# Optimization experiments

Hardware: AMD Instinct MI355X
Metric: run time of the kernel (lower is better)

The kernel has to match this reference:

```python
import jax, jax.numpy as jnp
import numpy as np

EMB = 2048
HEADS = 16


def setup_inputs() -> dict:
    key = jax.random.key(0)
    k_x, k_wqkv, k_bqkv, k_wo, k_bo = jax.random.split(key, 5)
    B, S, E = 2, 2048, EMB
    x = jax.random.normal(k_x, (B, S, E), dtype=jnp.float32)
    # nn.Linear weights stored as (in, out) for x @ W + b convention
    W_qkv = jax.random.normal(k_wqkv, (E, 3 * E), dtype=jnp.float32) * 0.02
    b_qkv = jax.random.normal(k_bqkv, (3 * E,), dtype=jnp.float32) * 0.02
    W_out = jax.random.normal(k_wo, (E, E), dtype=jnp.float32) * 0.02
    b_out = jax.random.normal(k_bo, (E,), dtype=jnp.float32) * 0.02
    return {"x": x, "W_qkv": W_qkv, "b_qkv": b_qkv, "W_out": W_out, "b_out": b_out}


def reference(x, W_qkv, b_qkv, W_out, b_out):
    B, S, E = x.shape
    H = HEADS
    dh = E // H
    # QKV projection: (B,S,3E)
    qkv = x @ W_qkv + b_qkv
    # Faithful to torch: reshape (B,S,H,3*dh) THEN split -> interleaved per-head q/k/v
    qkv = qkv.reshape(B, S, H, 3 * dh).transpose(0, 2, 1, 3)  # (B,H,S,3*dh)
    q, k, v = jnp.split(qkv, 3, axis=-1)  # each (B,H,S,dh)
    q = q / jnp.asarray(dh, q.dtype) ** 0.5
    scores = jnp.einsum('bhqd,bhkd->bhqk', q, k)  # (B,H,S,S)
    weights = jax.nn.softmax(scores, axis=-1)
    attn = jnp.einsum('bhqk,bhkd->bhqd', weights, v)  # (B,H,S,dh)
    attn = attn.transpose(0, 2, 1, 3).reshape(B, S, E)
    return attn @ W_out + b_out
```

## Files before the change

### kernel.cpp

```cpp
#include <hip/hip_runtime.h>
#include <type_traits>
#include <utility>

#define DI __device__ __forceinline__

typedef unsigned short u16;
typedef float f32x4 __attribute__((ext_vector_type(4)));
typedef float f32x16 __attribute__((ext_vector_type(16)));
typedef short s16x8 __attribute__((ext_vector_type(8)));
typedef __bf16 bf16x8 __attribute__((ext_vector_type(8)));

template <typename V, typename = void>
struct mfma_ok : std::false_type {};
template <typename V>
struct mfma_ok<V, std::void_t<decltype(__builtin_amdgcn_mfma_f32_16x16x32_bf16(
    std::declval<V>(), std::declval<V>(), std::declval<f32x4>(), 0, 0, 0))>>
    : std::true_type {};
using frag_t = std::conditional_t<mfma_ok<bf16x8>::value, bf16x8, s16x8>;

union U128 {
  int4 i;
  frag_t f;
  u16 s[8];
};

DI f32x4 mfma16(const U128& a, const U128& b, f32x4 c) {
  return __builtin_amdgcn_mfma_f32_16x16x32_bf16(a.f, b.f, c, 0, 0, 0);
}
DI f32x16 mfma32(const U128& a, const U128& b, f32x16 c) {
  return __builtin_amdgcn_mfma_f32_32x32x16_bf16(a.f, b.f, c, 0, 0, 0);
}

DI u16 f2b(float x) {
  union { float f; unsigned u; } v; v.f = x;
  unsigned r = v.u + 0x7FFFu + ((v.u >> 16) & 1u);
  return (u16)(r >> 16);
}

#if __has_builtin(__builtin_amdgcn_exp2f)
#define EXP2F __builtin_amdgcn_exp2f
#else
#define EXP2F exp2f
#endif

typedef __attribute__((address_space(1))) void gas_t;
typedef __attribute__((address_space(3))) void las_t;
DI void gll16(const void* g, void* l) {
  __builtin_amdgcn_global_load_lds((gas_t*)g, (las_t*)l, 16, 0, 0);
}

__global__ __launch_bounds__(256) void k_conv_bf16(const float* __restrict__ in,
                                                   u16* __restrict__ out, int n4) {
  int i = blockIdx.x * 256 + threadIdx.x;
  if (i >= n4) return;
  float4 v = ((const float4*)in)[i];
  ushort4 o;
  o.x = f2b(v.x); o.y = f2b(v.y); o.z = f2b(v.z); o.w = f2b(v.w);
  ((ushort4*)out)[i] = o;
}

__global__ __launch_bounds__(256) void k_transpose_f2b(const float* __restrict__ in,
                                                       u16* __restrict__ out,
                                                       int R, int C) {
  __shared__ __attribute__((aligned(16))) u16 Tb[64][68];
  int t = threadIdx.x;
  long r0 = (long)blockIdx.y * 64, c0 = (long)blockIdx.x * 64;
  int cq = (t & 15) * 4, rr = t >> 4;
#pragma unroll
  for (int it = 0; it < 4; ++it) {
    int r = rr + it * 16;
    float4 v = *(const float4*)(in + (r0 + r) * C + c0 + cq);
    Tb[r][cq + 0] = f2b(v.x); Tb[r][cq + 1] = f2b(v.y);
    Tb[r][cq + 2] = f2b(v.z); Tb[r][cq + 3] = f2b(v.w);
  }
  __syncthreads();
#pragma unroll
  for (int it = 0; it < 2; ++it) {
    int ci = it * 256 + t;
    int cc = ci >> 3, ch = ci & 7, rb = ch * 8;
    unsigned p0 = Tb[rb + 0][cc] | ((unsigned)Tb[rb + 1][cc] << 16);
    unsigned p1 = Tb[rb + 2][cc] | ((unsigned)Tb[rb + 3][cc] << 16);
    unsigned p2 = Tb[rb + 4][cc] | ((unsigned)Tb[rb + 5][cc] << 16);
    unsigned p3 = Tb[rb + 6][cc] | ((unsigned)Tb[rb + 7][cc] << 16);
    *(int4*)(out + (c0 + cc) * R + r0 + rb) = make_int4(p0, p1, p2, p3);
  }
}

template <bool BF16OUT>
__global__ __launch_bounds__(256) void k_gemm_bt(const u16* __restrict__ A,
                                                 const u16* __restrict__ Bt,
                                                 const float* __restrict__ bias,
                                                 void* __restrict__ Cout,
                                                 int M, int N, int K) {
  __shared__ __attribute__((aligned(16))) u16 As[128 * 32];
  __shared__ __attribute__((aligned(16))) u16 Bs[128 * 32];
  int t = threadIdx.x;
  int lane = t & 63, w = t >> 6, quad = lane >> 4, l15 = lane & 15;
  long m0 = (long)blockIdx.y * 128, n0 = (long)blockIdx.x * 128;
  int wr = (w >> 1) * 64, wc = (w & 1) * 64;
  f32x4 acc[4][4] = {};
  int ci0 = t, ci1 = t + 256;
  for (int k0 = 0; k0 < K; k0 += 32) {
    __syncthreads();
    gll16(A + (m0 + (ci0 >> 2)) * K + k0 + (ci0 & 3) * 8, As + ci0 * 8);
    gll16(A + (m0 + (ci1 >> 2)) * K + k0 + (ci1 & 3) * 8, As + ci1 * 8);
    gll16(Bt + (n0 + (ci0 >> 2)) * K + k0 + (ci0 & 3) * 8, Bs + ci0 * 8);
    gll16(Bt + (n0 + (ci1 >> 2)) * K + k0 + (ci1 & 3) * 8, Bs + ci1 * 8);
    __syncthreads();
    U128 a[4], b[4];
#pragma unroll
    for (int i = 0; i < 4; ++i)
      a[i].i = *(const int4*)(As + (wr + i * 16 + l15) * 32 + quad * 8);
#pragma unroll
    for (int j = 0; j < 4; ++j)
      b[j].i = *(const int4*)(Bs + (wc + j * 16 + l15) * 32 + quad * 8);
#pragma unroll
    for (int i = 0; i < 4; ++i)
#pragma unroll
      for (int j = 0; j < 4; ++j)
        acc[i][j] = mfma16(a[i], b[j], acc[i][j]);
  }
  float bj[4];
#pragma unroll
  for (int j = 0; j < 4; ++j) bj[j] = bias[n0 + wc + j * 16 + l15];
#pragma unroll
  for (int i = 0; i < 4; ++i) {
#pragma unroll
    for (int r = 0; r < 4; ++r) {
      long row = m0 + wr + i * 16 + quad * 4 + r;
#pragma unroll
      for (int j = 0; j < 4; ++j) {
        long col = n0 + wc + j * 16 + l15;
        float v = acc[i][j][r] + bj[j];
        if (BF16OUT) {
          unsigned pb = f2b(v);
          unsigned other = __shfl_xor(pb, 1);
          if (!(l15 & 1))
            ((unsigned*)Cout)[(row * N + col) >> 1] = pb | (other << 16);
        } else {
          ((float*)Cout)[row * N + col] = v;
        }
      }
    }
  }
}

__global__ __launch_bounds__(256) void k_extract_vt(const u16* __restrict__ qkv,
                                                    u16* __restrict__ vt) {
  __shared__ __attribute__((aligned(16))) u16 Vb[64][136];
  int t = threadIdx.x;
  int s0 = blockIdx.x * 64;
  int bh = blockIdx.y, b = bh >> 4, h = bh & 15;
  long rowbase = (long)b * 2048 + s0;
#pragma unroll
  for (int it = 0; it < 4; ++it) {
    int ci = it * 256 + t;
    int s = ci >> 4, ch = ci & 15;
    int4 v = *(const int4*)(qkv + (rowbase + s) * 6144 + h * 384 + 256 + ch * 8);
    *(int4*)(&Vb[s][ch * 8]) = v;
  }
  __syncthreads();
  long outbase = (long)bh * 128 * 2048 + s0;
#pragma unroll
  for (int it = 0; it < 4; ++it) {
    int ci = it * 256 + t;
    int d = ci >> 3, ch = ci & 7, sb = ch * 8;
    unsigned p0 = Vb[sb + 0][d] | ((unsigned)Vb[sb + 1][d] << 16);
    unsigned p1 = Vb[sb + 2][d] | ((unsigned)Vb[sb + 3][d] << 16);
    unsigned p2 = Vb[sb + 4][d] | ((unsigned)Vb[sb + 5][d] << 16);
    unsigned p3 = Vb[sb + 6][d] | ((unsigned)Vb[sb + 7][d] << 16);
    *(int4*)(vt + outbase + (long)d * 2048 + sb) = make_int4(p0, p1, p2, p3);
  }
}

__global__ __launch_bounds__(256, 2) void k_flash(const u16* __restrict__ qkv,
                                                  const u16* __restrict__ vt,
                                                  u16* __restrict__ attn) {
  __shared__ __attribute__((aligned(16))) u16 Ks[64 * 128];
  __shared__ __attribute__((aligned(16))) u16 Vts[128 * 64];
  int t = threadIdx.x;
  int lane = t & 63, w = t >> 6, l31 = lane & 31, h = lane >> 5;
  int q0 = blockIdx.x * 128 + w * 32;
  int bh = blockIdx.y, b = bh >> 4, hd = bh & 15;

  const u16* qbase = qkv + ((long)b * 2048 + q0 + l31) * 6144 + hd * 384;
  U128 qf[8];
#pragma unroll
  for (int dht = 0; dht < 8; ++dht)
    qf[dht].i = *(const int4*)(qbase + dht * 16 + h * 8);

  f32x16 O[4] = {};
  float lsum = 0.f;
  const float CEXP = 0.08838834764831845f * 1.4426950408889634f;
  long krowbase = (long)b * 2048;
  long vbase = (long)bh * 128 * 2048;

  for (int k0 = 0; k0 < 2048; k0 += 64) {
    __syncthreads();
#pragma unroll
    for (int it = 0; it < 4; ++it) {
      int ci = it * 256 + t;
      int key = ci >> 4, cp = ci & 15, cl = cp ^ (key & 7);
      gll16(qkv + (krowbase + k0 + key) * 6144 + hd * 384 + 128 + cl * 8, Ks + ci * 8);
    }
#pragma unroll
    for (int it = 0; it < 4; ++it) {
      int ci = it * 256 + t;
      int d = ci >> 3, cp = ci & 7, cl = cp ^ (d & 7);
      gll16(vt + vbase + (long)d * 2048 + k0 + cl * 8, Vts + ci * 8);
    }
    __syncthreads();

    f32x16 St[2] = {};
#pragma unroll
    for (int kb = 0; kb < 2; ++kb) {
      int row = kb * 32 + l31, sw = row & 7;
      const u16* kr = Ks + row * 128;
#pragma unroll
      for (int dht = 0; dht < 8; ++dht) {
        U128 kf;
        kf.i = *(const int4*)(kr + (((dht * 2 + h) ^ sw) << 3));
        St[kb] = mfma32(kf, qf[dht], St[kb]);
      }
    }

    float pk[2][16];
#pragma unroll
    for (int kb = 0; kb < 2; ++kb)
#pragma unroll
      for (int r = 0; r < 16; ++r) {
        float p = EXP2F(St[kb][r] * CEXP);
        pk[kb][r] = p;
        lsum += p;
      }

    U128 pf[4];
#pragma unroll
    for (int kb = 0; kb < 2; ++kb)
#pragma unroll
      for (int g = 0; g < 2; ++g) {
        float tmp[4], recv[4], lo[4], hi[4];
#pragma unroll
        for (int i = 0; i < 4; ++i)
          tmp[i] = h ? pk[kb][g * 8 + i] : pk[kb][g * 8 + 4 + i];
#pragma unroll
        for (int i = 0; i < 4; ++i) recv[i] = __shfl_xor(tmp[i], 32);
#pragma unroll
        for (int i = 0; i < 4; ++i) {
          lo[i] = h ? recv[i] : pk[kb][g * 8 + i];
          hi[i] = h ? pk[kb][g * 8 + 4 + i] : recv[i];
        }
        unsigned w0 = f2b(lo[0]) | ((unsigned)f2b(lo[1]) << 16);
        unsigned w1 = f2b(lo[2]) | ((unsigned)f2b(lo[3]) << 16);
        unsigned w2 = f2b(hi[0]) | ((unsigned)f2b(hi[1]) << 16);
        unsigned w3 = f2b(hi[2]) | ((unsigned)f2b(hi[3]) << 16);
        pf[kb * 2 + g].i = make_int4(w0, w1, w2, w3);
      }

#pragma unroll
    for (int kt = 0; kt < 4; ++kt)
#pragma unroll
      for (int dht = 0; dht < 4; ++dht) {
        int vrow = dht * 32 + l31, vsw = vrow & 7;
        U128 vf;
        vf.i = *(const int4*)(Vts + vrow * 64 + (((kt * 2 + h) ^ vsw) << 3));
        O[dht] = mfma32(vf, pf[kt], O[dht]);
      }
  }

  float ltot = lsum + __shfl_xor(lsum, 32);
  float inv = 1.f / ltot;
  long orow = (long)b * 2048 + q0 + l31;
  u16* ob = attn + orow * 2048 + hd * 128;
#pragma unroll
  for (int dht = 0; dht < 4; ++dht)
#pragma unroll
    for (int g = 0; g < 4; ++g) {
      int dh = dht * 32 + g * 8 + h * 4;
      float v0 = O[dht][4 * g + 0] * inv, v1 = O[dht][4 * g + 1] * inv;
      float v2 = O[dht][4 * g + 2] * inv, v3 = O[dht][4 * g + 3] * inv;
      uint2 pkd;
      pkd.x = f2b(v0) | ((unsigned)f2b(v1) << 16);
      pkd.y = f2b(v2) | ((unsigned)f2b(v3) << 16);
      *(uint2*)(ob + dh) = pkd;
    }
}

extern "C" void kernel_launch(void* const* d_in, const int* in_sizes, int n_in,
                              void* d_out, int out_size, void* d_ws, size_t ws_size,
                              hipStream_t stream) {
  const float* x    = (const float*)d_in[0];
  const float* Wqkv = (const float*)d_in[1];
  const float* bqkv = (const float*)d_in[2];
  const float* Wout = (const float*)d_in[3];
  const float* bout = (const float*)d_in[4];
  float* out = (float*)d_out;
  char* ws = (char*)d_ws;

  if (ws_size < 75497472u) return;

  u16* xb    = (u16*)d_out;
  u16* wqkvt = (u16*)(ws);
  u16* qkvb  = (u16*)(ws + 25165824);
  u16* woutt = (u16*)(ws);
  u16* attnb = (u16*)(ws + 8388608);
  u16* vtb   = (u16*)d_out;

  k_conv_bf16<<<8192, 256, 0, stream>>>(x, xb, 2097152);
  k_transpose_f2b<<<dim3(96, 32), 256, 0, stream>>>(Wqkv, wqkvt, 2048, 6144);
  k_gemm_bt<true><<<dim3(48, 32), 256, 0, stream>>>(xb, wqkvt, bqkv, qkvb, 4096, 6144, 2048);
  k_transpose_f2b<<<dim3(32, 32), 256, 0, stream>>>(Wout, woutt, 2048, 2048);
  k_extract_vt<<<dim3(32, 32), 256, 0, stream>>>(qkvb, vtb);
  k_flash<<<dim3(16, 32), 256, 0, stream>>>(qkvb, vtb, attnb);
  k_gemm_bt<false><<<dim3(16, 32), 256, 0, stream>>>(attnb, woutt, bout, out, 4096, 2048, 2048);
}
```

Before: 424.5 us.

## Deepen GEMM K-tile with swizzled LDS and stage contiguous per-head K buffer

```diff
diff --git a/kernel.cpp b/kernel.cpp
--- a/kernel.cpp
+++ b/kernel.cpp
@@ -87,38 +87,44 @@
 }
 
 template <bool BF16OUT>
-__global__ __launch_bounds__(256) void k_gemm_bt(const u16* __restrict__ A,
-                                                 const u16* __restrict__ Bt,
-                                                 const float* __restrict__ bias,
-                                                 void* __restrict__ Cout,
-                                                 int M, int N, int K) {
-  __shared__ __attribute__((aligned(16))) u16 As[128 * 32];
-  __shared__ __attribute__((aligned(16))) u16 Bs[128 * 32];
+__global__ __launch_bounds__(256, 4) void k_gemm_bt(const u16* __restrict__ A,
+                                                    const u16* __restrict__ Bt,
+                                                    const float* __restrict__ bias,
+                                                    void* __restrict__ Cout,
+                                                    int M, int N, int K) {
+  __shared__ __attribute__((aligned(16))) u16 As[128 * 64];
+  __shared__ __attribute__((aligned(16))) u16 Bs[128 * 64];
   int t = threadIdx.x;
   int lane = t & 63, w = t >> 6, quad = lane >> 4, l15 = lane & 15;
   long m0 = (long)blockIdx.y * 128, n0 = (long)blockIdx.x * 128;
   int wr = (w >> 1) * 64, wc = (w & 1) * 64;
+  int sw = l15 & 7;
   f32x4 acc[4][4] = {};
-  int ci0 = t, ci1 = t + 256;
-  for (int k0 = 0; k0 < K; k0 += 32) {
+  for (int k0 = 0; k0 < K; k0 += 64) {
     __syncthreads();
-    gll16(A + (m0 + (ci0 >> 2)) * K + k0 + (ci0 & 3) * 8, As + ci0 * 8);
-    gll16(A + (m0 + (ci1 >> 2)) * K + k0 + (ci1 & 3) * 8, As + ci1 * 8);
-    gll16(Bt + (n0 + (ci0 >> 2)) * K + k0 + (ci0 & 3) * 8, Bs + ci0 * 8);
-    gll16(Bt + (n0 + (ci1 >> 2)) * K + k0 + (ci1 & 3) * 8, Bs + ci1 * 8);
+#pragma unroll
+    for (int it = 0; it < 4; ++it) {
+      int ci = it * 256 + t;
+      int row = ci >> 3, cl = (ci & 7) ^ (row & 7);
+      gll16(A + (m0 + row) * K + k0 + cl * 8, As + ci * 8);
+      gll16(Bt + (n0 + row) * K + k0 + cl * 8, Bs + ci * 8);
+    }
     __syncthreads();
-    U128 a[4], b[4];
-#pragma unroll
-    for (int i = 0; i < 4; ++i)
-      a[i].i = *(const int4*)(As + (wr + i * 16 + l15) * 32 + quad * 8);
-#pragma unroll
-    for (int j = 0; j < 4; ++j)
-      b[j].i = *(const int4*)(Bs + (wc + j * 16 + l15) * 32 + quad * 8);
-#pragma unroll
-    for (int i = 0; i < 4; ++i)
+#pragma unroll
+    for (int kk = 0; kk < 2; ++kk) {
+      U128 a[4], b[4];
+#pragma unroll
+      for (int i = 0; i < 4; ++i)
+        a[i].i = *(const int4*)(As + (wr + i * 16 + l15) * 64 + (((kk * 4 + quad) ^ sw) << 3));
 #pragma unroll
       for (int j = 0; j < 4; ++j)
-        acc[i][j] = mfma16(a[i], b[j], acc[i][j]);
+        b[j].i = *(const int4*)(Bs + (wc + j * 16 + l15) * 64 + (((kk * 4 + quad) ^ sw) << 3));
+#pragma unroll
+      for (int i = 0; i < 4; ++i)
+#pragma unroll
+        for (int j = 0; j < 4; ++j)
+          acc[i][j] = mfma16(a[i], b[j], acc[i][j]);
+    }
   }
   float bj[4];
 #pragma unroll
@@ -145,13 +151,22 @@
   }
 }
 
-__global__ __launch_bounds__(256) void k_extract_vt(const u16* __restrict__ qkv,
-                                                    u16* __restrict__ vt) {
+__global__ __launch_bounds__(256) void k_extract_kvt(const u16* __restrict__ qkv,
+                                                     u16* __restrict__ kb,
+                                                     u16* __restrict__ vt) {
   __shared__ __attribute__((aligned(16))) u16 Vb[64][136];
   int t = threadIdx.x;
   int s0 = blockIdx.x * 64;
   int bh = blockIdx.y, b = bh >> 4, h = bh & 15;
   long rowbase = (long)b * 2048 + s0;
+  long krowout = (long)bh * 2048 + s0;
+#pragma unroll
+  for (int it = 0; it < 4; ++it) {
+    int ci = it * 256 + t;
+    int s = ci >> 4, ch = ci & 15;
+    int4 v = *(const int4*)(qkv + (rowbase + s) * 6144 + h * 384 + 128 + ch * 8);
+    *(int4*)(kb + (krowout + s) * 128 + ch * 8) = v;
+  }
 #pragma unroll
   for (int it = 0; it < 4; ++it) {
     int ci = it * 256 + t;
@@ -174,6 +189,7 @@
 }
 
 __global__ __launch_bounds__(256, 2) void k_flash(const u16* __restrict__ qkv,
+                                                  const u16* __restrict__ kb,
                                                   const u16* __restrict__ vt,
                                                   u16* __restrict__ attn) {
   __shared__ __attribute__((aligned(16))) u16 Ks[64 * 128];
@@ -192,7 +208,7 @@
   f32x16 O[4] = {};
   float lsum = 0.f;
   const float CEXP = 0.08838834764831845f * 1.4426950408889634f;
-  long krowbase = (long)b * 2048;
+  const u16* kbh = kb + (long)bh * 2048 * 128;
   long vbase = (long)bh * 128 * 2048;
 
   for (int k0 = 0; k0 < 2048; k0 += 64) {
@@ -201,7 +217,7 @@
     for (int it = 0; it < 4; ++it) {
       int ci = it * 256 + t;
       int key = ci >> 4, cp = ci & 15, cl = cp ^ (key & 7);
-      gll16(qkv + (krowbase + k0 + key) * 6144 + hd * 384 + 128 + cl * 8, Ks + ci * 8);
+      gll16(kbh + (k0 + key) * 128 + cl * 8, Ks + ci * 8);
     }
 #pragma unroll
     for (int it = 0; it < 4; ++it) {
@@ -213,48 +229,48 @@
 
     f32x16 St[2] = {};
 #pragma unroll
-    for (int kb = 0; kb < 2; ++kb) {
-      int row = kb * 32 + l31, sw = row & 7;
+    for (int kb2 = 0; kb2 < 2; ++kb2) {
+      int row = kb2 * 32 + l31, sw = row & 7;
       const u16* kr = Ks + row * 128;
 #pragma unroll
       for (int dht = 0; dht < 8; ++dht) {
         U128 kf;
         kf.i = *(const int4*)(kr + (((dht * 2 + h) ^ sw) << 3));
-        St[kb] = mfma32(kf, qf[dht], St[kb]);
+        St[kb2] = mfma32(kf, qf[dht], St[kb2]);
       }
     }
 
     float pk[2][16];
 #pragma unroll
-    for (int kb = 0; kb < 2; ++kb)
+    for (int kb2 = 0; kb2 < 2; ++kb2)
 #pragma unroll
       for (int r = 0; r < 16; ++r) {
-        float p = EXP2F(St[kb][r] * CEXP);
-        pk[kb][r] = p;
+        float p = EXP2F(St[kb2][r] * CEXP);
+        pk[kb2][r] = p;
         lsum += p;
       }
 
     U128 pf[4];
 #pragma unroll
-    for (int kb = 0; kb < 2; ++kb)
+    for (int kb2 = 0; kb2 < 2; ++kb2)
 #pragma unroll
       for (int g = 0; g < 2; ++g) {
         float tmp[4], recv[4], lo[4], hi[4];
 #pragma unroll
         for (int i = 0; i < 4; ++i)
-          tmp[i] = h ? pk[kb][g * 8 + i] : pk[kb][g * 8 + 4 + i];
+          tmp[i] = h ? pk[kb2][g * 8 + i] : pk[kb2][g * 8 + 4 + i];
 #pragma unroll
         for (int i = 0; i < 4; ++i) recv[i] = __shfl_xor(tmp[i], 32);
 #pragma unroll
         for (int i = 0; i < 4; ++i) {
-          lo[i] = h ? recv[i] : pk[kb][g * 8 + i];
-          hi[i] = h ? pk[kb][g * 8 + 4 + i] : recv[i];
+          lo[i] = h ? recv[i] : pk[kb2][g * 8 + i];
+          hi[i] = h ? pk[kb2][g * 8 + 4 + i] : recv[i];
         }
         unsigned w0 = f2b(lo[0]) | ((unsigned)f2b(lo[1]) << 16);
         unsigned w1 = f2b(lo[2]) | ((unsigned)f2b(lo[3]) << 16);
         unsigned w2 = f2b(hi[0]) | ((unsigned)f2b(hi[1]) << 16);
         unsigned w3 = f2b(hi[2]) | ((unsigned)f2b(hi[3]) << 16);
-        pf[kb * 2 + g].i = make_int4(w0, w1, w2, w3);
+        pf[kb2 * 2 + g].i = make_int4(w0, w1, w2, w3);
       }
 
 #pragma unroll
@@ -302,15 +318,16 @@
   u16* xb    = (u16*)d_out;
   u16* wqkvt = (u16*)(ws);
   u16* qkvb  = (u16*)(ws + 25165824);
+  u16* vtb   = (u16*)d_out;
+  u16* kbuf  = (u16*)((char*)d_out + 16777216);
   u16* woutt = (u16*)(ws);
   u16* attnb = (u16*)(ws + 8388608);
-  u16* vtb   = (u16*)d_out;
 
   k_conv_bf16<<<8192, 256, 0, stream>>>(x, xb, 2097152);
   k_transpose_f2b<<<dim3(96, 32), 256, 0, stream>>>(Wqkv, wqkvt, 2048, 6144);
   k_gemm_bt<true><<<dim3(48, 32), 256, 0, stream>>>(xb, wqkvt, bqkv, qkvb, 4096, 6144, 2048);
+  k_extract_kvt<<<dim3(32, 32), 256, 0, stream>>>(qkvb, kbuf, vtb);
   k_transpose_f2b<<<dim3(32, 32), 256, 0, stream>>>(Wout, woutt, 2048, 2048);
-  k_extract_vt<<<dim3(32, 32), 256, 0, stream>>>(qkvb, vtb);
-  k_flash<<<dim3(16, 32), 256, 0, stream>>>(qkvb, vtb, attnb);
+  k_flash<<<dim3(16, 32), 256, 0, stream>>>(qkvb, kbuf, vtb, attnb);
   k_gemm_bt<false><<<dim3(16, 32), 256, 0, stream>>>(attnb, woutt, bout, out, 4096, 2048, 2048);
 }
```

Result: faster. 398.0 us (-6.3%).
